# Kernel tuning notes

Measured on AMD Instinct MI355X. Metric: run time of the kernel, lower is better.

The kernel has to match this reference:

```python
import jax, jax.numpy as jnp
import numpy as np

NEG_INF = -1e30


def setup_inputs() -> dict:
    key = jax.random.key(0)
    ks = jax.random.split(key, 5)
    B, S, D, H = 2, 2048, 1024, 16
    sc = 0.02  # weight init scale
    return {
        "x": jax.random.normal(ks[0], (B, S, D), dtype=jnp.float32),
        "Wq": jax.random.normal(ks[1], (D, D), dtype=jnp.float32) * sc,
        "bq": jnp.zeros((D,), dtype=jnp.float32),
        "Wk": jax.random.normal(ks[2], (D, D), dtype=jnp.float32) * sc,
        "bk": jnp.zeros((D,), dtype=jnp.float32),
        "Wv": jax.random.normal(ks[3], (D, D), dtype=jnp.float32) * sc,
        "bv": jnp.zeros((D,), dtype=jnp.float32),
        "Wo": jax.random.normal(ks[4], (D, D), dtype=jnp.float32) * sc,
        "bo": jnp.zeros((D,), dtype=jnp.float32),
        "temperature": jnp.ones((H,), dtype=jnp.float32),
    }


def reference(x, Wq, bq, Wk, bk, Wv, bv, Wo, bo, temperature):
    B, S, D = x.shape
    H = temperature.shape[0]
    hd = D // H
    sparsity = 0.8
    k = max(1, int(S * (1.0 - sparsity)))
    scale = hd ** (-0.5)

    # torch Linear: y = x @ W^T + b ; reshape to [B, S, H, hd] -> [B, H, S, hd]
    def proj(W, b):
        return (x @ W.T + b).reshape(B, S, H, hd).transpose(0, 2, 1, 3)

    q, kk, v = proj(Wq, bq), proj(Wk, bk), proj(Wv, bv)

    temp = jnp.clip(temperature, 0.1, None)[None, :, None, None]  # [1,H,1,1]
    scores = jnp.einsum("bhqd,bhkd->bhqk", q, kk) * scale / temp  # [B,H,S,S]

    # top-k sparsity: keep the k largest scores per row, -inf elsewhere.
    # Equivalent to torch's topk+scatter for distinct values: threshold at
    # the k-th largest value per row.
    topk_vals = jax.lax.top_k(scores, k)[0]           # [B,H,S,k]
    kth = topk_vals[..., -1:]                          # [B,H,S,1]
    sparse_scores = jnp.where(scores >= kth, scores, NEG_INF)

    attn = jax.nn.softmax(sparse_scores, axis=-1)      # [B,H,S,S]
    head_out = jnp.einsum("bhqk,bhkd->bhqd", attn, v)  # [B,H,S,hd]

    # stack heads back: [B,S,H,hd] -> [B,S,D], then out projection
    out = head_out.transpose(0, 2, 1, 3).reshape(B, S, D)
    out = out @ Wo.T + bo

    avg_attention = attn.mean(axis=1)                  # [B,S,S]
    return out, avg_attention
```

## Files before the change

kernel.cpp:

```cpp
#include <hip/hip_runtime.h>
#include <stdint.h>

#define S_LEN 2048
#define D_DIM 1024
#define NHEAD 16
#define HD    64
#define TOPK  409

typedef unsigned short u16;
typedef __attribute__((ext_vector_type(8))) short bf16x8;
typedef __attribute__((ext_vector_type(4))) float f32x4;
#define MFMA __builtin_amdgcn_mfma_f32_16x16x32_bf16

__device__ __forceinline__ u16 f2b(float f) {
    unsigned u = __float_as_uint(f);
    return (u16)((u + 0x7fffu + ((u >> 16) & 1u)) >> 16);
}
__device__ __forceinline__ float b2f(u16 h) {
    return __uint_as_float(((unsigned)h) << 16);
}

__global__ __launch_bounds__(256, 4)
void split_f32(const float* __restrict__ src, u16* __restrict__ hi,
               u16* __restrict__ lo, int n4)
{
    const int i = blockIdx.x * 256 + threadIdx.x;
    if (i >= n4) return;
    const float4 v = ((const float4*)src)[i];
    const float vv[4] = {v.x, v.y, v.z, v.w};
    u16 h4[4], l4[4];
#pragma unroll
    for (int c = 0; c < 4; ++c) {
        h4[c] = f2b(vv[c]);
        l4[c] = f2b(vv[c] - b2f(h4[c]));
    }
    ((ushort4*)hi)[i] = make_ushort4(h4[0], h4[1], h4[2], h4[3]);
    ((ushort4*)lo)[i] = make_ushort4(l4[0], l4[1], l4[2], l4[3]);
}

__global__ __launch_bounds__(256, 4)
void zero_f32(float* __restrict__ p, int n4)
{
    const int i = blockIdx.x * 256 + threadIdx.x;
    if (i < n4) ((float4*)p)[i] = make_float4(0.f, 0.f, 0.f, 0.f);
}

template<int MODE>
__global__ __launch_bounds__(512, 2)
void proj_mfma(const u16* __restrict__ Ahi, const u16* __restrict__ Alo,
               const u16* __restrict__ Whi, const u16* __restrict__ Wlo,
               const float* __restrict__ bias, float* __restrict__ outf,
               u16* __restrict__ o1, u16* __restrict__ o2)
{
    const int t = threadIdx.x, w = t >> 6, l = t & 63;
    const int lq = l & 15, quad = l >> 4;
    const int m0 = blockIdx.y * 128 + (w >> 2) * 64;
    const int n0 = blockIdx.x * 128 + (w & 3) * 32;

    f32x4 acc[4][2];
#pragma unroll
    for (int i = 0; i < 4; ++i)
#pragma unroll
        for (int j = 0; j < 2; ++j) acc[i][j] = (f32x4){0.f, 0.f, 0.f, 0.f};

    const size_t abase = (size_t)(m0 + lq) * D_DIM + quad * 8;
    const size_t bbase = (size_t)(n0 + lq) * D_DIM + quad * 8;

#pragma unroll 2
    for (int k0 = 0; k0 < D_DIM; k0 += 32) {
        bf16x8 ah[4], al[4], bh[2], bl[2];
#pragma unroll
        for (int i = 0; i < 4; ++i) {
            ah[i] = *(const bf16x8*)(Ahi + abase + (size_t)i * 16 * D_DIM + k0);
            al[i] = *(const bf16x8*)(Alo + abase + (size_t)i * 16 * D_DIM + k0);
        }
#pragma unroll
        for (int j = 0; j < 2; ++j) {
            bh[j] = *(const bf16x8*)(Whi + bbase + (size_t)j * 16 * D_DIM + k0);
            bl[j] = *(const bf16x8*)(Wlo + bbase + (size_t)j * 16 * D_DIM + k0);
        }
#pragma unroll
        for (int i = 0; i < 4; ++i)
#pragma unroll
            for (int j = 0; j < 2; ++j) {
                acc[i][j] = MFMA(ah[i], bh[j], acc[i][j], 0, 0, 0);
                acc[i][j] = MFMA(ah[i], bl[j], acc[i][j], 0, 0, 0);
                acc[i][j] = MFMA(al[i], bh[j], acc[i][j], 0, 0, 0);
            }
    }

#pragma unroll
    for (int j = 0; j < 2; ++j) {
        const int n = n0 + j * 16 + lq;
        const float bb = bias[n];
        const int hh = n >> 6, ee = n & 63;
#pragma unroll
        for (int i = 0; i < 4; ++i) {
            const int mb = m0 + i * 16 + quad * 4;
            const int bbm = mb >> 11, ss = mb & 2047;
            if (MODE == 2) {
#pragma unroll
                for (int r = 0; r < 4; ++r)
                    outf[(size_t)(mb + r) * D_DIM + n] = acc[i][j][r] + bb;
            } else if (MODE == 1) {
                ushort4 pk;
                pk.x = f2b(acc[i][j][0] + bb);
                pk.y = f2b(acc[i][j][1] + bb);
                pk.z = f2b(acc[i][j][2] + bb);
                pk.w = f2b(acc[i][j][3] + bb);
                *(ushort4*)(o1 + ((size_t)((bbm * NHEAD + hh) * HD + ee)) * S_LEN + ss) = pk;
            } else {
#pragma unroll
                for (int r = 0; r < 4; ++r) {
                    const float v = acc[i][j][r] + bb;
                    const size_t idx = ((size_t)(bbm * NHEAD + hh) * S_LEN + ss + r) * HD + ee;
                    const u16 h = f2b(v);
                    o1[idx] = h;
                    o2[idx] = f2b(v - b2f(h));
                }
            }
        }
    }
}

__global__ __launch_bounds__(512, 2)
void attn_mfma(const u16* __restrict__ Qhi, const u16* __restrict__ Qlo,
               const u16* __restrict__ Khi, const u16* __restrict__ Klo,
               const u16* __restrict__ Vt,  const float* __restrict__ temp,
               u16* __restrict__ HOhi, u16* __restrict__ HOlo,
               float* __restrict__ avg)
{
    __shared__ __align__(16) u16 aLds[16 * 2056];
    __shared__ float pvpart[4 * 16 * 16];
    __shared__ int   cnts[16][8][5];
    __shared__ float red[16][8][2];
    __shared__ float rowMu[16], rowSig[16], rowLo[16], rowHi[16], rowZi[16];

    const int t = threadIdx.x, w = t >> 6, l = t & 63;
    const int lq = l & 15, quad = l >> 4;
    const int b  = blockIdx.x >> 7;
    const int q0 = (blockIdx.x & 127) << 4;
    const int h0 = blockIdx.y << 3;

    float avgreg[64];
#pragma unroll
    for (int i = 0; i < 64; ++i) avgreg[i] = 0.f;

#pragma unroll 1
    for (int hh = 0; hh < 8; ++hh) {
        const int h = h0 + hh;
        const size_t bh = (size_t)(b * NHEAD + h) * S_LEN;
        const float tscale = 0.125f / fmaxf(temp[h], 0.1f);

        const u16* qph = Qhi + (bh + q0 + lq) * HD + quad * 8;
        const u16* qpl = Qlo + (bh + q0 + lq) * HD + quad * 8;
        const bf16x8 qh0 = *(const bf16x8*)qph;
        const bf16x8 qh1 = *(const bf16x8*)(qph + 32);
        const bf16x8 ql0 = *(const bf16x8*)qpl;
        const bf16x8 ql1 = *(const bf16x8*)(qpl + 32);

        f32x4 acc[16];
        const u16* kph = Khi + (bh + w * 256 + lq) * HD + quad * 8;
        const u16* kpl = Klo + (bh + w * 256 + lq) * HD + quad * 8;
#pragma unroll
        for (int tt = 0; tt < 16; ++tt) {
            const bf16x8 k0 = *(const bf16x8*)(kph + tt * 16 * HD);
            const bf16x8 k1 = *(const bf16x8*)(kph + tt * 16 * HD + 32);
            const bf16x8 m0 = *(const bf16x8*)(kpl + tt * 16 * HD);
            const bf16x8 m1 = *(const bf16x8*)(kpl + tt * 16 * HD + 32);
            f32x4 a = {0.f, 0.f, 0.f, 0.f};
            a = MFMA(qh0, k0, a, 0, 0, 0);
            a = MFMA(qh1, k1, a, 0, 0, 0);
            a = MFMA(qh0, m0, a, 0, 0, 0);
            a = MFMA(qh1, m1, a, 0, 0, 0);
            a = MFMA(ql0, k0, a, 0, 0, 0);
            a = MFMA(ql1, k1, a, 0, 0, 0);
            acc[tt] = a * tscale;
        }
        __syncthreads();

        {
            float s1[4] = {0.f,0.f,0.f,0.f}, s2[4] = {0.f,0.f,0.f,0.f};
#pragma unroll
            for (int tt = 0; tt < 16; ++tt)
#pragma unroll
                for (int r = 0; r < 4; ++r) {
                    const float v = acc[tt][r];
                    s1[r] += v;
                    s2[r] = __fmaf_rn(v, v, s2[r]);
                }
#pragma unroll
            for (int off = 1; off < 16; off <<= 1)
#pragma unroll
                for (int r = 0; r < 4; ++r) {
                    s1[r] += __shfl_xor(s1[r], off, 16);
                    s2[r] += __shfl_xor(s2[r], off, 16);
                }
            if (lq == 0)
#pragma unroll
                for (int r = 0; r < 4; ++r) {
                    red[quad * 4 + r][w][0] = s1[r];
                    red[quad * 4 + r][w][1] = s2[r];
                }
        }
        __syncthreads();
        if (t < 16) {
            float a = 0.f, c = 0.f;
#pragma unroll
            for (int ww = 0; ww < 8; ++ww) { a += red[t][ww][0]; c += red[t][ww][1]; }
            const float mu = a * (1.f / 2048.f);
            const float va = c * (1.f / 2048.f) - mu * mu;
            rowMu[t] = mu;
            rowSig[t] = sqrtf(fmaxf(va, 0.f));
        }
        __syncthreads();

        {
            float th[5][4];
            int c[5][4];
#pragma unroll
            for (int r = 0; r < 4; ++r) {
                const float mu = rowMu[quad * 4 + r], sg = rowSig[quad * 4 + r];
#pragma unroll
                for (int i = 0; i < 5; ++i) {
                    th[i][r] = __fmaf_rn(sg, 0.55f + 0.15f * (float)i, mu);
                    c[i][r] = 0;
                }
            }
#pragma unroll
            for (int tt = 0; tt < 16; ++tt)
#pragma unroll
                for (int r = 0; r < 4; ++r) {
                    const float v = acc[tt][r];
#pragma unroll
                    for (int i = 0; i < 5; ++i) c[i][r] += (v >= th[i][r]) ? 1 : 0;
                }
#pragma unroll
            for (int off = 1; off < 16; off <<= 1)
#pragma unroll
                for (int i = 0; i < 5; ++i)
#pragma unroll
                    for (int r = 0; r < 4; ++r) c[i][r] += __shfl_xor(c[i][r], off, 16);
            if (lq == 0)
#pragma unroll
                for (int r = 0; r < 4; ++r)
#pragma unroll
                    for (int i = 0; i < 5; ++i) cnts[quad * 4 + r][w][i] = c[i][r];
        }
        __syncthreads();
        if (t < 16) {
            int c[5] = {0, 0, 0, 0, 0};
#pragma unroll
            for (int ww = 0; ww < 8; ++ww)
#pragma unroll
                for (int i = 0; i < 5; ++i) c[i] += cnts[t][ww][i];
            const float mu = rowMu[t], sg = rowSig[t];
            float lo, hi;
            if (c[0] < TOPK) {
                lo = __fmaf_rn(sg, -6.f, mu);
                hi = __fmaf_rn(sg, 0.55f + 0.15f * 0.f, mu);
            } else if (c[4] >= TOPK) {
                lo = __fmaf_rn(sg, 0.55f + 0.15f * 4.f, mu);
                hi = __fmaf_rn(sg, 6.f, mu);
            } else {
                int bi = 0;
#pragma unroll
                for (int j = 1; j < 4; ++j) if (c[j] >= TOPK) bi = j;
                lo = __fmaf_rn(sg, 0.55f + 0.15f * (float)bi, mu);
                hi = __fmaf_rn(sg, 0.55f + 0.15f * (float)(bi + 1), mu);
            }
            rowLo[t] = lo;
            rowHi[t] = hi;
        }
        __syncthreads();

#pragma unroll 1
        for (int rd = 0; rd < 5; ++rd) {
            {
                float th[3][4];
                int c[3][4];
#pragma unroll
                for (int r = 0; r < 4; ++r) {
                    const float lo_ = rowLo[quad * 4 + r], hi_ = rowHi[quad * 4 + r];
                    const float w4 = __fmul_rn(__fsub_rn(hi_, lo_), 0.25f);
#pragma unroll
                    for (int j = 0; j < 3; ++j) {
                        th[j][r] = __fmaf_rn(w4, (float)(j + 1), lo_);
                        c[j][r] = 0;
                    }
                }
#pragma unroll
                for (int tt = 0; tt < 16; ++tt)
#pragma unroll
                    for (int r = 0; r < 4; ++r) {
                        const float v = acc[tt][r];
#pragma unroll
                        for (int j = 0; j < 3; ++j) c[j][r] += (v >= th[j][r]) ? 1 : 0;
                    }
#pragma unroll
                for (int off = 1; off < 16; off <<= 1)
#pragma unroll
                    for (int j = 0; j < 3; ++j)
#pragma unroll
                        for (int r = 0; r < 4; ++r) c[j][r] += __shfl_xor(c[j][r], off, 16);
                if (lq == 0)
#pragma unroll
                    for (int r = 0; r < 4; ++r)
#pragma unroll
                        for (int j = 0; j < 3; ++j) cnts[quad * 4 + r][w][j] = c[j][r];
            }
            __syncthreads();
            if (t < 16) {
                int d[3] = {0, 0, 0};
#pragma unroll
                for (int ww = 0; ww < 8; ++ww)
#pragma unroll
                    for (int j = 0; j < 3; ++j) d[j] += cnts[t][ww][j];
                float lo = rowLo[t], hi = rowHi[t];
                const float w4 = __fmul_rn(__fsub_rn(hi, lo), 0.25f);
                const float t1 = __fmaf_rn(w4, 1.f, lo);
                const float t2 = __fmaf_rn(w4, 2.f, lo);
                const float t3 = __fmaf_rn(w4, 3.f, lo);
                if (d[2] >= TOPK)      { lo = t3; }
                else if (d[1] >= TOPK) { lo = t2; hi = t3; }
                else if (d[0] >= TOPK) { lo = t1; hi = t2; }
                else                   { hi = t1; }
                rowLo[t] = lo;
                rowHi[t] = hi;
            }
            __syncthreads();
        }

        float kth[4], zp[4] = {0.f, 0.f, 0.f, 0.f};
#pragma unroll
        for (int r = 0; r < 4; ++r) kth[r] = rowLo[quad * 4 + r];
#pragma unroll
        for (int tt = 0; tt < 16; ++tt)
#pragma unroll
            for (int r = 0; r < 4; ++r) {
                const float v = acc[tt][r];
                const float e = (v >= kth[r]) ? __expf(v) : 0.f;
                acc[tt][r] = e;
                zp[r] += e;
            }
#pragma unroll
        for (int off = 1; off < 16; off <<= 1)
#pragma unroll
            for (int r = 0; r < 4; ++r) zp[r] += __shfl_xor(zp[r], off, 16);
        if (lq == 0)
#pragma unroll
            for (int r = 0; r < 4; ++r) red[quad * 4 + r][w][0] = zp[r];
        __syncthreads();
        if (t < 16) {
            float z = 0.f;
#pragma unroll
            for (int ww = 0; ww < 8; ++ww) z += red[t][ww][0];
            rowZi[t] = 1.f / z;
        }
        __syncthreads();
        float zi[4];
#pragma unroll
        for (int r = 0; r < 4; ++r) zi[r] = rowZi[quad * 4 + r];

#pragma unroll
        for (int tt = 0; tt < 16; ++tt)
#pragma unroll
            for (int r = 0; r < 4; ++r) {
                const float a_ = acc[tt][r] * zi[r];
                avgreg[tt * 4 + r] += a_;
                aLds[(quad * 4 + r) * 2056 + w * 256 + tt * 16 + lq] = f2b(a_);
            }
        __syncthreads();

        const int et = w & 3, jh = w >> 2;
        const u16* vb = Vt + ((size_t)(b * NHEAD + h) * HD + et * 16 + lq) * S_LEN
                        + jh * 1024 + quad * 8;
        const u16* ab = aLds + lq * 2056 + jh * 1024 + quad * 8;
        f32x4 pv = {0.f, 0.f, 0.f, 0.f};
#pragma unroll 8
        for (int st = 0; st < 32; ++st) {
            const bf16x8 af = *(const bf16x8*)(ab + st * 32);
            const bf16x8 vf = *(const bf16x8*)(vb + st * 32);
            pv = MFMA(af, vf, pv, 0, 0, 0);
        }
        if (w >= 4) {
#pragma unroll
            for (int r = 0; r < 4; ++r)
                pvpart[(et * 16 + quad * 4 + r) * 16 + lq] = pv[r];
        }
        __syncthreads();
        if (w < 4) {
#pragma unroll
            for (int r = 0; r < 4; ++r) {
                const float v = pv[r] + pvpart[(et * 16 + quad * 4 + r) * 16 + lq];
                const size_t idx =
                    ((size_t)(b * S_LEN + q0 + quad * 4 + r)) * D_DIM + h * HD + et * 16 + lq;
                const u16 hv = f2b(v);
                HOhi[idx] = hv;
                HOlo[idx] = f2b(v - b2f(hv));
            }
        }
    }

#pragma unroll
    for (int tt = 0; tt < 16; ++tt)
#pragma unroll
        for (int r = 0; r < 4; ++r)
            atomicAdd(&avg[((size_t)(b * S_LEN + q0 + quad * 4 + r)) * S_LEN
                           + w * 256 + tt * 16 + lq],
                      avgreg[tt * 4 + r] * (1.f / NHEAD));
}

extern "C" void kernel_launch(void* const* d_in, const int* in_sizes, int n_in,
                              void* d_out, int out_size, void* d_ws, size_t ws_size,
                              hipStream_t stream)
{
    const float* x    = (const float*)d_in[0];
    const float* Wq   = (const float*)d_in[1];
    const float* bq   = (const float*)d_in[2];
    const float* Wk   = (const float*)d_in[3];
    const float* bk   = (const float*)d_in[4];
    const float* Wv   = (const float*)d_in[5];
    const float* bv   = (const float*)d_in[6];
    const float* Wo   = (const float*)d_in[7];
    const float* bo   = (const float*)d_in[8];
    const float* temp = (const float*)d_in[9];
    float* out = (float*)d_out;

    const int B = in_sizes[0] / (S_LEN * D_DIM);
    const int M = B * S_LEN;
    const size_t NQ = (size_t)M * D_DIM;
    const size_t NW = (size_t)D_DIM * D_DIM;

    u16* Qhi = (u16*)d_ws;
    u16* Qlo = Qhi + NQ;
    u16* Khi = Qlo + NQ;
    u16* Klo = Khi + NQ;
    u16* Vt  = Klo + NQ;
    u16* Xhi = Vt  + NQ;
    u16* Xlo = Xhi + NQ;
    u16* Wqh = Xlo + NQ;
    u16* Wql = Wqh + NW;
    u16* Wkh = Wql + NW;
    u16* Wkl = Wkh + NW;
    u16* Wvh = Wkl + NW;
    u16* Wvl = Wvh + NW;
    u16* Woh = Wvl + NW;
    u16* Wol = Woh + NW;
    float* avg = out + NQ;

    const int n4x = (int)(NQ / 4), n4w = (int)(NW / 4);
    const int n4a = (int)((size_t)M * S_LEN / 4);
    zero_f32<<<(n4a + 255) / 256, 256, 0, stream>>>(avg, n4a);
    split_f32<<<(n4x + 255) / 256, 256, 0, stream>>>(x,  Xhi, Xlo, n4x);
    split_f32<<<(n4w + 255) / 256, 256, 0, stream>>>(Wq, Wqh, Wql, n4w);
    split_f32<<<(n4w + 255) / 256, 256, 0, stream>>>(Wk, Wkh, Wkl, n4w);
    split_f32<<<(n4w + 255) / 256, 256, 0, stream>>>(Wv, Wvh, Wvl, n4w);
    split_f32<<<(n4w + 255) / 256, 256, 0, stream>>>(Wo, Woh, Wol, n4w);

    dim3 gg(D_DIM / 128, M / 128, 1);
    proj_mfma<0><<<gg, 512, 0, stream>>>(Xhi, Xlo, Wqh, Wql, bq, nullptr, Qhi, Qlo);
    proj_mfma<0><<<gg, 512, 0, stream>>>(Xhi, Xlo, Wkh, Wkl, bk, nullptr, Khi, Klo);
    proj_mfma<1><<<gg, 512, 0, stream>>>(Xhi, Xlo, Wvh, Wvl, bv, nullptr, Vt, nullptr);

    attn_mfma<<<dim3(M / 16, 2), 512, 0, stream>>>(Qhi, Qlo, Khi, Klo, Vt, temp,
                                                   Xhi, Xlo, avg);

    proj_mfma<2><<<gg, 512, 0, stream>>>(Xhi, Xlo, Woh, Wol, bo, out, nullptr, nullptr);
}
```

Baseline: 1.226 ms.

## Pack per-head attention average into fp16 pairs to raise attention kernel occupancy

The 64-float per-thread accumulator for the head-averaged attention map is replaced by 32 packed fp16x2 registers built with round-toward-zero conversion. The launch bound is raised from 2 to 4 blocks per CU. The reduction and counting loops are reordered to process one row at a time, and the QK loop unroll is cut to 8, both to lower register pressure. This trades accuracy of the averaged attention output (fp16 accumulation with truncation over 8 heads) for more resident waves, and may cause spills if the register budget is not met.

Measured after the change: 2.520 ms. 2.06x slower.

```diff
diff --git a/kernel.cpp b/kernel.cpp
--- a/kernel.cpp
+++ b/kernel.cpp
@@ -10,6 +10,7 @@
 typedef unsigned short u16;
 typedef __attribute__((ext_vector_type(8))) short bf16x8;
 typedef __attribute__((ext_vector_type(4))) float f32x4;
+typedef __attribute__((ext_vector_type(2))) __fp16 f16x2;
 #define MFMA __builtin_amdgcn_mfma_f32_16x16x32_bf16
 
 __device__ __forceinline__ u16 f2b(float f) {
@@ -123,7 +124,7 @@
     }
 }
 
-__global__ __launch_bounds__(512, 2)
+__global__ __launch_bounds__(512, 4)
 void attn_mfma(const u16* __restrict__ Qhi, const u16* __restrict__ Qlo,
                const u16* __restrict__ Khi, const u16* __restrict__ Klo,
                const u16* __restrict__ Vt,  const float* __restrict__ temp,
@@ -142,9 +143,9 @@
     const int q0 = (blockIdx.x & 127) << 4;
     const int h0 = blockIdx.y << 3;
 
-    float avgreg[64];
-#pragma unroll
-    for (int i = 0; i < 64; ++i) avgreg[i] = 0.f;
+    f16x2 avgpk[32];
+#pragma unroll
+    for (int i = 0; i < 32; ++i) avgpk[i] = (f16x2){(__fp16)0.f, (__fp16)0.f};
 
 #pragma unroll 1
     for (int hh = 0; hh < 8; ++hh) {
@@ -162,7 +163,7 @@
         f32x4 acc[16];
         const u16* kph = Khi + (bh + w * 256 + lq) * HD + quad * 8;
         const u16* kpl = Klo + (bh + w * 256 + lq) * HD + quad * 8;
-#pragma unroll
+#pragma unroll 8
         for (int tt = 0; tt < 16; ++tt) {
             const bf16x8 k0 = *(const bf16x8*)(kph + tt * 16 * HD);
             const bf16x8 k1 = *(const bf16x8*)(kph + tt * 16 * HD + 32);
@@ -180,28 +181,25 @@
         __syncthreads();
 
         {
-            float s1[4] = {0.f,0.f,0.f,0.f}, s2[4] = {0.f,0.f,0.f,0.f};
-#pragma unroll
-            for (int tt = 0; tt < 16; ++tt)
-#pragma unroll
-                for (int r = 0; r < 4; ++r) {
+#pragma unroll
+            for (int r = 0; r < 4; ++r) {
+                float s1 = 0.f, s2 = 0.f;
+#pragma unroll
+                for (int tt = 0; tt < 16; ++tt) {
                     const float v = acc[tt][r];
-                    s1[r] += v;
-                    s2[r] = __fmaf_rn(v, v, s2[r]);
-                }
-#pragma unroll
-            for (int off = 1; off < 16; off <<= 1)
-#pragma unroll
-                for (int r = 0; r < 4; ++r) {
-                    s1[r] += __shfl_xor(s1[r], off, 16);
-                    s2[r] += __shfl_xor(s2[r], off, 16);
-                }
-            if (lq == 0)
-#pragma unroll
-                for (int r = 0; r < 4; ++r) {
-                    red[quad * 4 + r][w][0] = s1[r];
-                    red[quad * 4 + r][w][1] = s2[r];
-                }
+                    s1 += v;
+                    s2 = __fmaf_rn(v, v, s2);
+                }
+#pragma unroll
+                for (int off = 1; off < 16; off <<= 1) {
+                    s1 += __shfl_xor(s1, off, 16);
+                    s2 += __shfl_xor(s2, off, 16);
+                }
+                if (lq == 0) {
+                    red[quad * 4 + r][w][0] = s1;
+                    red[quad * 4 + r][w][1] = s2;
+                }
+            }
         }
         __syncthreads();
         if (t < 16) {
@@ -216,36 +214,30 @@
         __syncthreads();
 
         {
-            float th[5][4];
-            int c[5][4];
 #pragma unroll
             for (int r = 0; r < 4; ++r) {
                 const float mu = rowMu[quad * 4 + r], sg = rowSig[quad * 4 + r];
+                float th[5];
+                int c[5];
 #pragma unroll
                 for (int i = 0; i < 5; ++i) {
-                    th[i][r] = __fmaf_rn(sg, 0.55f + 0.15f * (float)i, mu);
-                    c[i][r] = 0;
-                }
-            }
-#pragma unroll
-            for (int tt = 0; tt < 16; ++tt)
-#pragma unroll
-                for (int r = 0; r < 4; ++r) {
+                    th[i] = __fmaf_rn(sg, 0.55f + 0.15f * (float)i, mu);
+                    c[i] = 0;
+                }
+#pragma unroll
+                for (int tt = 0; tt < 16; ++tt) {
                     const float v = acc[tt][r];
 #pragma unroll
-                    for (int i = 0; i < 5; ++i) c[i][r] += (v >= th[i][r]) ? 1 : 0;
-                }
-#pragma unroll
-            for (int off = 1; off < 16; off <<= 1)
-#pragma unroll
-                for (int i = 0; i < 5; ++i)
-#pragma unroll
-                    for (int r = 0; r < 4; ++r) c[i][r] += __shfl_xor(c[i][r], off, 16);
-            if (lq == 0)
-#pragma unroll
-                for (int r = 0; r < 4; ++r)
-#pragma unroll
-                    for (int i = 0; i < 5; ++i) cnts[quad * 4 + r][w][i] = c[i][r];
+                    for (int i = 0; i < 5; ++i) c[i] += (v >= th[i]) ? 1 : 0;
+                }
+#pragma unroll
+                for (int off = 1; off < 16; off <<= 1)
+#pragma unroll
+                    for (int i = 0; i < 5; ++i) c[i] += __shfl_xor(c[i], off, 16);
+                if (lq == 0)
+#pragma unroll
+                    for (int i = 0; i < 5; ++i) cnts[quad * 4 + r][w][i] = c[i];
+            }
         }
         __syncthreads();
         if (t < 16) {
@@ -277,37 +269,31 @@
 #pragma unroll 1
         for (int rd = 0; rd < 5; ++rd) {
             {
-                float th[3][4];
-                int c[3][4];
 #pragma unroll
                 for (int r = 0; r < 4; ++r) {
                     const float lo_ = rowLo[quad * 4 + r], hi_ = rowHi[quad * 4 + r];
                     const float w4 = __fmul_rn(__fsub_rn(hi_, lo_), 0.25f);
+                    float th[3];
+                    int c[3];
 #pragma unroll
                     for (int j = 0; j < 3; ++j) {
-                        th[j][r] = __fmaf_rn(w4, (float)(j + 1), lo_);
-                        c[j][r] = 0;
+                        th[j] = __fmaf_rn(w4, (float)(j + 1), lo_);
+                        c[j] = 0;
                     }
-                }
-#pragma unroll
-                for (int tt = 0; tt < 16; ++tt)
-#pragma unroll
-                    for (int r = 0; r < 4; ++r) {
+#pragma unroll
+                    for (int tt = 0; tt < 16; ++tt) {
                         const float v = acc[tt][r];
 #pragma unroll
-                        for (int j = 0; j < 3; ++j) c[j][r] += (v >= th[j][r]) ? 1 : 0;
+                        for (int j = 0; j < 3; ++j) c[j] += (v >= th[j]) ? 1 : 0;
                     }
 #pragma unroll
-                for (int off = 1; off < 16; off <<= 1)
-#pragma unroll
-                    for (int j = 0; j < 3; ++j)
-#pragma unroll
-                        for (int r = 0; r < 4; ++r) c[j][r] += __shfl_xor(c[j][r], off, 16);
-                if (lq == 0)
-#pragma unroll
-                    for (int r = 0; r < 4; ++r)
-#pragma unroll
-                        for (int j = 0; j < 3; ++j) cnts[quad * 4 + r][w][j] = c[j][r];
+                    for (int off = 1; off < 16; off <<= 1)
+#pragma unroll
+                        for (int j = 0; j < 3; ++j) c[j] += __shfl_xor(c[j], off, 16);
+                    if (lq == 0)
+#pragma unroll
+                        for (int j = 0; j < 3; ++j) cnts[quad * 4 + r][w][j] = c[j];
+                }
             }
             __syncthreads();
             if (t < 16) {
@@ -363,13 +349,20 @@
         for (int r = 0; r < 4; ++r) zi[r] = rowZi[quad * 4 + r];
 
 #pragma unroll
-        for (int tt = 0; tt < 16; ++tt)
+        for (int tt = 0; tt < 16; ++tt) {
+            float a_[4];
 #pragma unroll
             for (int r = 0; r < 4; ++r) {
-                const float a_ = acc[tt][r] * zi[r];
-                avgreg[tt * 4 + r] += a_;
-                aLds[(quad * 4 + r) * 2056 + w * 256 + tt * 16 + lq] = f2b(a_);
-            }
+                a_[r] = acc[tt][r] * zi[r];
+                aLds[(quad * 4 + r) * 2056 + w * 256 + tt * 16 + lq] = f2b(a_[r]);
+            }
+            const f16x2 p0 = avgpk[tt * 2 + 0];
+            const f16x2 p1 = avgpk[tt * 2 + 1];
+            avgpk[tt * 2 + 0] =
+                __builtin_amdgcn_cvt_pkrtz((float)p0[0] + a_[0], (float)p0[1] + a_[1]);
+            avgpk[tt * 2 + 1] =
+                __builtin_amdgcn_cvt_pkrtz((float)p1[0] + a_[2], (float)p1[1] + a_[3]);
+        }
         __syncthreads();
 
         const int et = w & 3, jh = w >> 2;
@@ -403,12 +396,16 @@
     }
 
 #pragma unroll
-    for (int tt = 0; tt < 16; ++tt)
+    for (int tt = 0; tt < 16; ++tt) {
+        const f16x2 p0 = avgpk[tt * 2 + 0];
+        const f16x2 p1 = avgpk[tt * 2 + 1];
+        const float vals[4] = {(float)p0[0], (float)p0[1], (float)p1[0], (float)p1[1]};
 #pragma unroll
         for (int r = 0; r < 4; ++r)
             atomicAdd(&avg[((size_t)(b * S_LEN + q0 + quad * 4 + r)) * S_LEN
                            + w * 256 + tt * 16 + lq],
-                      avgreg[tt * 4 + r] * (1.f / NHEAD));
+                      vals[r] * (1.f / NHEAD));
+    }
 }
 
 extern "C" void kernel_launch(void* const* d_in, const int* in_sizes, int n_in,
```
